# Optimization experiments

Hardware: AMD Instinct MI355X
Metric: run time of the kernel (lower is better)

Reference implementation:

```python
import jax, jax.numpy as jnp
import numpy as np

B, S, H, HEADS = 4, 4096, 256, 4
DH = H // HEADS
WINDOW = 16
N = B * S
EPS = 1e-5


def _build_edges():
    half = WINDOW // 2
    i = np.arange(S)
    offs = np.concatenate([np.arange(-half, 0), np.arange(1, half)])  # j in [i-half, i+half), j != i
    j = i[:, None] + offs[None, :]
    valid = (j >= 0) & (j < S)
    src_i = np.broadcast_to(i[:, None], j.shape)[valid]
    tgt_j = j[valid]
    w = (1.0 / (1.0 + np.abs(src_i - tgt_j))).astype(np.float32)
    boff = np.arange(B)[:, None] * S
    src = (boff + src_i[None, :]).reshape(-1).astype(np.int32)
    tgt = (boff + tgt_j[None, :]).reshape(-1).astype(np.int32)
    w = np.tile(w, B)
    return src, tgt, w


def setup_inputs() -> dict:
    key = jax.random.key(0)
    ks = jax.random.split(key, 8)
    src, tgt, w = _build_edges()
    sc = 0.02
    return {
        "hidden_states": jax.random.normal(ks[0], (B, S, H), jnp.float32),
        "Wc": jax.random.normal(ks[1], (H, H), jnp.float32) * sc,
        "bc": jnp.zeros((H,), jnp.float32),
        "Wa": jax.random.normal(ks[2], (H, H), jnp.float32) * sc,
        "a_src": jax.random.normal(ks[3], (HEADS, DH), jnp.float32) * sc,
        "a_tgt": jax.random.normal(ks[4], (HEADS, DH), jnp.float32) * sc,
        "ba": jnp.zeros((H,), jnp.float32),
        "ln_g": jnp.ones((H,), jnp.float32),
        "ln_b": jnp.zeros((H,), jnp.float32),
        "Wg": jax.random.normal(ks[5], (2 * H, H), jnp.float32) * sc,
        "bg": jnp.zeros((H,), jnp.float32),
        "Wp": jax.random.normal(ks[6], (H, H), jnp.float32) * sc,
        "bp": jnp.zeros((H,), jnp.float32),
        "edge_weights": jnp.asarray(w),
        "src": jnp.asarray(src),
        "tgt": jnp.asarray(tgt),
    }


def _ln(x, g, b):
    mu = jnp.mean(x, -1, keepdims=True)
    var = jnp.mean((x - mu) ** 2, -1, keepdims=True)
    return (x - mu) * jax.lax.rsqrt(var + EPS) * g + b


def reference(hidden_states, Wc, bc, Wa, a_src, a_tgt, ba, ln_g, ln_b,
              Wg, bg, Wp, bp, edge_weights, src, tgt):
    x = hidden_states.reshape(N, H)

    # --- layer 0: GraphConvolution ---
    support = x @ Wc                                   # [N,H]
    msg = edge_weights[:, None] * support[src]         # [E,H]
    gs = jax.ops.segment_sum(msg, tgt, num_segments=N) + bc
    gs = _ln(gs + x, ln_g, ln_b)

    # --- layer 1: GraphAttention (GAT-style, edge-weighted softmax) ---
    h = (gs @ Wa).reshape(N, HEADS, DH)
    es = jnp.einsum('nhd,hd->nh', h, a_src)            # [N,heads]
    et = jnp.einsum('nhd,hd->nh', h, a_tgt)
    logits = jax.nn.leaky_relu(es[src] + et[tgt], 0.2)  # [E,heads]
    m = jax.ops.segment_max(logits, tgt, num_segments=N)
    un = jnp.exp(logits - m[tgt]) * edge_weights[:, None]
    den = jax.ops.segment_sum(un, tgt, num_segments=N)
    alpha = un / (den[tgt] + 1e-9)                      # [E,heads]
    agg = jax.ops.segment_sum(alpha[:, :, None] * h[src], tgt, num_segments=N)
    gs = agg.reshape(N, H) + ba
    gs = _ln(gs + x, ln_g, ln_b)

    # --- gated integration ---
    gate = jax.nn.sigmoid(jnp.concatenate([x, gs], -1) @ Wg + bg)
    enhanced = x + gate * (gs @ Wp + bp)
    return enhanced.reshape(B, S, H)
```

## Files before the change

kernel.cpp:

```cpp
#include <hip/hip_runtime.h>
#include <math.h>

#define HD 256
#define SEQ 4096
#define NR 16384
#define NHEADS 4
#define EPSV 1e-5f
#define LDP 72
#define SROWS 32
#define SHALO 15
#define SLDP 264

typedef __attribute__((ext_vector_type(8))) short bf16x8;
typedef __attribute__((ext_vector_type(4))) float f32x4;

__device__ inline short f2bf(float f) {
    unsigned u = __float_as_uint(f);
    u += 0x7FFF + ((u >> 16) & 1);
    return (short)(u >> 16);
}
__device__ inline float bf2f(short s) {
    return __uint_as_float(((unsigned)(unsigned short)s) << 16);
}

__device__ inline void stage_tile(const short* __restrict__ src, int src_stride,
                                  int row0, int k0, short* lds, int rows)
{
    int t = threadIdx.x;
    int nchunk = rows >> 5;
#pragma unroll
    for (int c = 0; c < 4; ++c) {
        if (c >= nchunk) break;
        int idx = c * 256 + t;
        int r = idx >> 3, kg = idx & 7;
        bf16x8 v = *(const bf16x8*)(src + (size_t)(row0 + r) * src_stride + k0 + kg * 8);
        *(bf16x8*)(lds + r * LDP + kg * 8) = v;
    }
}

__device__ inline void stage_tile_ln(const short* __restrict__ z, int row0, int k0,
                                     const float* __restrict__ musum,
                                     const float* __restrict__ sqsum,
                                     const float* __restrict__ g,
                                     const float* __restrict__ b,
                                     short* lds, int rows)
{
    int t = threadIdx.x;
    int nchunk = rows >> 5;
#pragma unroll
    for (int c = 0; c < 4; ++c) {
        if (c >= nchunk) break;
        int idx = c * 256 + t;
        int r = idx >> 3, kg = idx & 7;
        int row = row0 + r;
        float s = musum[row], q = sqsum[row];
        float mu = s * (1.f / HD);
        float inv = rsqrtf(q * (1.f / HD) - mu * mu + EPSV);
        bf16x8 v = *(const bf16x8*)(z + (size_t)row * HD + k0 + kg * 8);
        float4 g0 = *(const float4*)(g + k0 + kg * 8);
        float4 g1 = *(const float4*)(g + k0 + kg * 8 + 4);
        float4 b0 = *(const float4*)(b + k0 + kg * 8);
        float4 b1 = *(const float4*)(b + k0 + kg * 8 + 4);
        bf16x8 o;
        o[0] = f2bf((bf2f(v[0]) - mu) * inv * g0.x + b0.x);
        o[1] = f2bf((bf2f(v[1]) - mu) * inv * g0.y + b0.y);
        o[2] = f2bf((bf2f(v[2]) - mu) * inv * g0.z + b0.z);
        o[3] = f2bf((bf2f(v[3]) - mu) * inv * g0.w + b0.w);
        o[4] = f2bf((bf2f(v[4]) - mu) * inv * g1.x + b1.x);
        o[5] = f2bf((bf2f(v[5]) - mu) * inv * g1.y + b1.y);
        o[6] = f2bf((bf2f(v[6]) - mu) * inv * g1.z + b1.z);
        o[7] = f2bf((bf2f(v[7]) - mu) * inv * g1.w + b1.w);
        *(bf16x8*)(lds + r * LDP + kg * 8) = o;
    }
}

__global__ __launch_bounds__(256) void prep_stencil(
    const float* __restrict__ x,
    const float* __restrict__ Wc, const float* __restrict__ Wa,
    const float* __restrict__ Wg, const float* __restrict__ Wp,
    short* __restrict__ xb, short* __restrict__ y,
    short* __restrict__ WcT, short* __restrict__ WaT,
    short* __restrict__ WgT, short* __restrict__ WpT,
    float* __restrict__ musum, float* __restrict__ sqsum)
{
    __shared__ __align__(16) char smem[(SROWS + SHALO) * SLDP * 2];
    int task = blockIdx.y;
    int bx = blockIdx.x;
    int t = threadIdx.x;

    if (task == 0) {
        short* lH = (short*)smem;
        int t0 = bx * SROWS;
        int batch_base = t0 & ~(SEQ - 1);
        for (int i = t; i < (SROWS + SHALO) * 64; i += 256) {
            int r = i >> 6, c4 = (i & 63) * 4;
            int grow = t0 - 7 + r;
            short4 o4 = {0, 0, 0, 0};
            if (grow >= batch_base && grow < batch_base + SEQ) {
                float4 v = *(const float4*)(x + (size_t)grow * HD + c4);
                o4.x = f2bf(v.x); o4.y = f2bf(v.y); o4.z = f2bf(v.z); o4.w = f2bf(v.w);
            }
            *(short4*)(lH + r * SLDP + c4) = o4;
        }
        __syncthreads();
        for (int i = t; i < SROWS * 64; i += 256) {
            int r = i >> 6, c4 = (i & 63) * 4;
            *(short4*)(xb + (size_t)(t0 + r) * HD + c4) =
                *(const short4*)(lH + (r + 7) * SLDP + c4);
        }
        int wv = t >> 6, lane = t & 63;
        int c0 = lane * 4;
        for (int rr = wv; rr < SROWS; rr += 4) {
            float a0 = 0.f, a1 = 0.f, a2 = 0.f, a3 = 0.f;
#pragma unroll
            for (int i = 0; i < 15; ++i) {
                int d = (i < 7) ? (i - 7) : (i - 6);
                float wd = 1.f / (1.f + (float)((d < 0) ? -d : d));
                short4 s4 = *(const short4*)(lH + (rr + 7 + d) * SLDP + c0);
                a0 += wd * bf2f(s4.x); a1 += wd * bf2f(s4.y);
                a2 += wd * bf2f(s4.z); a3 += wd * bf2f(s4.w);
            }
            short4 o;
            o.x = f2bf(a0); o.y = f2bf(a1); o.z = f2bf(a2); o.w = f2bf(a3);
            *(short4*)(y + (size_t)(t0 + rr) * HD + c0) = o;
        }
        return;
    }
    if (task == 5) {
        int idx = bx * 256 + t;
        if (idx < NR) { musum[idx] = 0.f; sqsum[idx] = 0.f; }
        return;
    }
    float (*lds)[65] = (float (*)[65])smem;
    const float* W; short* Wt; int K;
    if (task == 1)      { W = Wc; Wt = WcT; K = 256; }
    else if (task == 2) { W = Wa; Wt = WaT; K = 256; }
    else if (task == 3) { W = Wg; Wt = WgT; K = 512; }
    else                { W = Wp; Wt = WpT; K = 256; }
    int ntiles = (K >> 6) * 4;
    if (bx >= ntiles) return;
    int k0 = (bx >> 2) * 64, n0 = (bx & 3) * 64;
    int ty = t >> 6, tx = t & 63;
#pragma unroll
    for (int s = 0; s < 16; ++s) {
        int r = s * 4 + ty;
        lds[r][tx] = W[(size_t)(k0 + r) * 256 + n0 + tx];
    }
    __syncthreads();
#pragma unroll
    for (int s = 0; s < 16; ++s) {
        int rn = s * 4 + ty;
        Wt[(size_t)(n0 + rn) * K + k0 + tx] = f2bf(lds[tx][rn]);
    }
}

__global__ __launch_bounds__(256) void gemm1z(const short* __restrict__ A,
                                              const short* __restrict__ BT,
                                              const short* __restrict__ xb,
                                              const float* __restrict__ bc,
                                              short* __restrict__ Z,
                                              float* __restrict__ musum,
                                              float* __restrict__ sqsum)
{
    __shared__ __align__(16) short lA[64 * LDP];
    __shared__ __align__(16) short lB[64 * LDP];
    int tid = threadIdx.x;
    int lane = tid & 63, wid = tid >> 6;
    int m0 = blockIdx.y * 64;
    int n0 = blockIdx.x * 64;
    int wrow = wid * 16;
    int lm = lane & 15, lk = (lane >> 4) * 8;
    f32x4 acc[4] = {};
    for (int kt = 0; kt < 4; ++kt) {
        __syncthreads();
        stage_tile(A,  HD, m0, kt * 64, lA, 64);
        stage_tile(BT, HD, n0, kt * 64, lB, 64);
        __syncthreads();
#pragma unroll
        for (int kk2 = 0; kk2 < 64; kk2 += 32) {
            bf16x8 a = *(const bf16x8*)(lA + (wrow + lm) * LDP + kk2 + lk);
            bf16x8 b[4];
#pragma unroll
            for (int j = 0; j < 4; ++j)
                b[j] = *(const bf16x8*)(lB + (j * 16 + lm) * LDP + kk2 + lk);
#pragma unroll
            for (int j = 0; j < 4; ++j)
                acc[j] = __builtin_amdgcn_mfma_f32_16x16x32_bf16(a, b[j], acc[j], 0, 0, 0);
        }
    }
    int rbase = (lane >> 4) * 4;
#pragma unroll
    for (int r = 0; r < 4; ++r) {
        int row = m0 + wrow + rbase + r;
        float s = 0.f, q = 0.f;
#pragma unroll
        for (int j = 0; j < 4; ++j) {
            int n = n0 + j * 16 + lm;
            float z = acc[j][r] + bc[n] + bf2f(xb[(size_t)row * HD + n]);
            Z[(size_t)row * HD + n] = f2bf(z);
            s += z; q += z * z;
        }
#pragma unroll
        for (int o = 1; o < 16; o <<= 1) {
            s += __shfl_xor(s, o, 64);
            q += __shfl_xor(q, o, 64);
        }
        if (lm == 0) {
            atomicAdd(&musum[row], s);
            atomicAdd(&sqsum[row], q);
        }
    }
}

__global__ __launch_bounds__(256) void gemm_dots2(const short* __restrict__ Z,
                                                  const short* __restrict__ BT,
                                                  const float* __restrict__ musum,
                                                  const float* __restrict__ sqsum,
                                                  const float* __restrict__ lng,
                                                  const float* __restrict__ lnb,
                                                  const float* __restrict__ a_src,
                                                  const float* __restrict__ a_tgt,
                                                  short* __restrict__ C,
                                                  float* __restrict__ es,
                                                  float* __restrict__ et)
{
    __shared__ __align__(16) short lA[64 * LDP];
    __shared__ __align__(16) short lB[64 * LDP];
    int tid = threadIdx.x;
    int lane = tid & 63, wid = tid >> 6;
    int m0 = blockIdx.y * 64;
    int n0 = blockIdx.x * 64;
    int wrow = wid * 16;
    int lm = lane & 15, lk = (lane >> 4) * 8;
    f32x4 acc[4] = {};
    for (int kt = 0; kt < 4; ++kt) {
        __syncthreads();
        stage_tile_ln(Z, m0, kt * 64, musum, sqsum, lng, lnb, lA, 64);
        stage_tile(BT, HD, n0, kt * 64, lB, 64);
        __syncthreads();
#pragma unroll
        for (int kk2 = 0; kk2 < 64; kk2 += 32) {
            bf16x8 a = *(const bf16x8*)(lA + (wrow + lm) * LDP + kk2 + lk);
            bf16x8 b[4];
#pragma unroll
            for (int j = 0; j < 4; ++j)
                b[j] = *(const bf16x8*)(lB + (j * 16 + lm) * LDP + kk2 + lk);
#pragma unroll
            for (int j = 0; j < 4; ++j)
                acc[j] = __builtin_amdgcn_mfma_f32_16x16x32_bf16(a, b[j], acc[j], 0, 0, 0);
        }
    }
    int rbase = (lane >> 4) * 4;
#pragma unroll
    for (int j = 0; j < 4; ++j)
#pragma unroll
        for (int r = 0; r < 4; ++r)
            C[(size_t)(m0 + wrow + rbase + r) * HD + n0 + j * 16 + lm] = f2bf(acc[j][r]);

    float as4[4], at4[4];
#pragma unroll
    for (int j = 0; j < 4; ++j) {
        as4[j] = a_src[n0 + j * 16 + lm];
        at4[j] = a_tgt[n0 + j * 16 + lm];
    }
#pragma unroll
    for (int r = 0; r < 4; ++r) {
        float ps = 0.f, pt = 0.f;
#pragma unroll
        for (int j = 0; j < 4; ++j) {
            ps += acc[j][r] * as4[j];
            pt += acc[j][r] * at4[j];
        }
#pragma unroll
        for (int o = 1; o < 16; o <<= 1) {
            ps += __shfl_xor(ps, o, 64);
            pt += __shfl_xor(pt, o, 64);
        }
        if (lm == 0) {
            int row = m0 + wrow + rbase + r;
            es[row * NHEADS + blockIdx.x] = ps;
            et[row * NHEADS + blockIdx.x] = pt;
        }
    }
}

__global__ __launch_bounds__(256) void attn_ln(const short* __restrict__ hb,
                                               const float* __restrict__ es,
                                               const float* __restrict__ et,
                                               const short* __restrict__ xb,
                                               const float* __restrict__ ba,
                                               const float* __restrict__ g,
                                               const float* __restrict__ bb,
                                               short* __restrict__ out)
{
    __shared__ short lH[(SROWS + SHALO) * SLDP];
    int t0 = blockIdx.x * SROWS;
    int batch_base = t0 & ~(SEQ - 1);
    int t = threadIdx.x;
    for (int i = t; i < (SROWS + SHALO) * 64; i += 256) {
        int r = i >> 6, c4 = (i & 63) * 4;
        int grow = t0 - 7 + r;
        short4 v = {0, 0, 0, 0};
        if (grow >= batch_base && grow < batch_base + SEQ)
            v = *(const short4*)(hb + (size_t)grow * HD + c4);
        *(short4*)(lH + r * SLDP + c4) = v;
    }
    __syncthreads();

    int wv = t >> 6, lane = t & 63;
    int tap = lane >> 2, hh = lane & 3;
    int hd = lane >> 4;
    int c0 = lane * 4;
    for (int rr = wv; rr < SROWS; rr += 4) {
        int trow = t0 + rr;
        int p = trow & (SEQ - 1);
        float lg = -1e30f, wd = 0.f;
        bool okk = false;
        if (tap < 15) {
            int d = (tap < 7) ? (tap - 7) : (tap - 6);
            int qp = p + d;
            okk = (qp >= 0) && (qp < SEQ);
            if (okk) {
                float l = es[(trow + d) * NHEADS + hh] + et[trow * NHEADS + hh];
                lg = (l > 0.f) ? l : 0.2f * l;
            }
            wd = 1.f / (1.f + (float)((d < 0) ? -d : d));
        }
        float m = lg;
#pragma unroll
        for (int o = 4; o < 64; o <<= 1) m = fmaxf(m, __shfl_xor(m, o, 64));
        float un = okk ? __expf(lg - m) * wd : 0.f;
        float den = un;
#pragma unroll
        for (int o = 4; o < 64; o <<= 1) den += __shfl_xor(den, o, 64);
        float alpha_l = un / (den + 1e-9f);

        float al[15];
#pragma unroll
        for (int i = 0; i < 15; ++i) al[i] = __shfl(alpha_l, i * 4 + hd, 64);

        float a0 = 0.f, a1 = 0.f, a2 = 0.f, a3 = 0.f;
#pragma unroll
        for (int i = 0; i < 15; ++i) {
            int d = (i < 7) ? (i - 7) : (i - 6);
            short4 s4 = *(const short4*)(lH + (rr + 7 + d) * SLDP + c0);
            a0 += al[i] * bf2f(s4.x); a1 += al[i] * bf2f(s4.y);
            a2 += al[i] * bf2f(s4.z); a3 += al[i] * bf2f(s4.w);
        }
        short4 xv4 = *(const short4*)(xb + (size_t)trow * HD + c0);
        float4 bav = *(const float4*)(ba + c0);
        float v0 = a0 + bav.x + bf2f(xv4.x), v1 = a1 + bav.y + bf2f(xv4.y);
        float v2 = a2 + bav.z + bf2f(xv4.z), v3 = a3 + bav.w + bf2f(xv4.w);
        float s = v0 + v1 + v2 + v3;
        float q = v0 * v0 + v1 * v1 + v2 * v2 + v3 * v3;
#pragma unroll
        for (int o = 1; o < 64; o <<= 1) { s += __shfl_xor(s, o, 64); q += __shfl_xor(q, o, 64); }
        float mu = s * (1.f / HD);
        float var = q * (1.f / HD) - mu * mu;
        float inv = rsqrtf(var + EPSV);
        float4 gv = *(const float4*)(g + c0);
        float4 bv = *(const float4*)(bb + c0);
        short4 o4;
        o4.x = f2bf((v0 - mu) * inv * gv.x + bv.x);
        o4.y = f2bf((v1 - mu) * inv * gv.y + bv.y);
        o4.z = f2bf((v2 - mu) * inv * gv.z + bv.z);
        o4.w = f2bf((v3 - mu) * inv * gv.w + bv.w);
        *(short4*)(out + (size_t)trow * HD + c0) = o4;
    }
}

__global__ __launch_bounds__(256) void final_mfma(const short* __restrict__ xb,
                                                  const short* __restrict__ gs2b,
                                                  const short* __restrict__ WgT,
                                                  const float* __restrict__ bg,
                                                  const short* __restrict__ WpT,
                                                  const float* __restrict__ bp,
                                                  float* __restrict__ out)
{
    __shared__ __align__(16) short lX[64 * LDP];
    __shared__ __align__(16) short lG[64 * LDP];
    __shared__ __align__(16) short lB1[64 * LDP];
    __shared__ __align__(16) short lB2[64 * LDP];
    __shared__ __align__(16) short lB3[64 * LDP];
    int tid = threadIdx.x;
    int lane = tid & 63, wid = tid >> 6;
    int m0 = blockIdx.y * 64;
    int n0 = blockIdx.x * 64;
    int wrow = wid * 16;
    int lm = lane & 15, lk = (lane >> 4) * 8;
    f32x4 accg[4] = {}, accp[4] = {};
    for (int kt = 0; kt < 4; ++kt) {
        int k0 = kt * 64;
        __syncthreads();
        stage_tile(xb,   HD,  m0, k0, lX, 64);
        stage_tile(gs2b, HD,  m0, k0, lG, 64);
        stage_tile(WgT,  512, n0, k0, lB1, 64);
        stage_tile(WgT,  512, n0, k0 + 256, lB2, 64);
        stage_tile(WpT,  HD,  n0, k0, lB3, 64);
        __syncthreads();
#pragma unroll
        for (int kk2 = 0; kk2 < 64; kk2 += 32) {
            int ro = (wrow + lm) * LDP + kk2 + lk;
            bf16x8 ax = *(const bf16x8*)(lX + ro);
            bf16x8 ag = *(const bf16x8*)(lG + ro);
            bf16x8 b1[4], b2[4], b3[4];
#pragma unroll
            for (int j = 0; j < 4; ++j) {
                int rb = (j * 16 + lm) * LDP + kk2 + lk;
                b1[j] = *(const bf16x8*)(lB1 + rb);
                b2[j] = *(const bf16x8*)(lB2 + rb);
                b3[j] = *(const bf16x8*)(lB3 + rb);
            }
#pragma unroll
            for (int j = 0; j < 4; ++j) {
                accg[j] = __builtin_amdgcn_mfma_f32_16x16x32_bf16(ax, b1[j], accg[j], 0, 0, 0);
                accg[j] = __builtin_amdgcn_mfma_f32_16x16x32_bf16(ag, b2[j], accg[j], 0, 0, 0);
                accp[j] = __builtin_amdgcn_mfma_f32_16x16x32_bf16(ag, b3[j], accp[j], 0, 0, 0);
            }
        }
    }
    int rbase = (lane >> 4) * 4;
#pragma unroll
    for (int j = 0; j < 4; ++j)
#pragma unroll
        for (int r = 0; r < 4; ++r) {
            size_t m = (size_t)(m0 + wrow + rbase + r);
            int n = n0 + j * 16 + lm;
            float gate = 1.f / (1.f + __expf(-(accg[j][r] + bg[n])));
            float pv = accp[j][r] + bp[n];
            out[m * HD + n] = bf2f(xb[m * HD + n]) + gate * pv;
        }
}

extern "C" void kernel_launch(void* const* d_in, const int* in_sizes, int n_in,
                              void* d_out, int out_size, void* d_ws, size_t ws_size,
                              hipStream_t stream)
{
    const float* x     = (const float*)d_in[0];
    const float* Wc    = (const float*)d_in[1];
    const float* bc    = (const float*)d_in[2];
    const float* Wa    = (const float*)d_in[3];
    const float* a_src = (const float*)d_in[4];
    const float* a_tgt = (const float*)d_in[5];
    const float* ba    = (const float*)d_in[6];
    const float* ln_g  = (const float*)d_in[7];
    const float* ln_b  = (const float*)d_in[8];
    const float* Wg    = (const float*)d_in[9];
    const float* bg    = (const float*)d_in[10];
    const float* Wp    = (const float*)d_in[11];
    const float* bp    = (const float*)d_in[12];

    float* out = (float*)d_out;
    short* hb  = (short*)d_out;
    char* dsec = (char*)d_out + (size_t)NR * HD * 2;
    float* es  = (float*)dsec;
    float* et  = es + (size_t)NR * NHEADS;

    char* w = (char*)d_ws;
    short* y   = (short*)w;   w += (size_t)NR * HD * 2;
    short* zb  = (short*)w;   w += (size_t)NR * HD * 2;
    short* xb  = (short*)w;   w += (size_t)NR * HD * 2;
    short* WcT = (short*)w;   w += 256 * 256 * 2;
    short* WaT = (short*)w;   w += 256 * 256 * 2;
    short* WpT = (short*)w;   w += 256 * 256 * 2;
    short* WgT = (short*)w;   w += 512 * 256 * 2;
    float* musum = (float*)w; w += (size_t)NR * 4;
    float* sqsum = (float*)w; w += (size_t)NR * 4;

    dim3 ggrid(HD / 64, NR / 64);

    prep_stencil<<<dim3(NR / SROWS, 6), 256, 0, stream>>>(
        x, Wc, Wa, Wg, Wp, xb, y, WcT, WaT, WgT, WpT, musum, sqsum);
    gemm1z<<<ggrid, 256, 0, stream>>>(y, WcT, xb, bc, zb, musum, sqsum);
    gemm_dots2<<<ggrid, 256, 0, stream>>>(zb, WaT, musum, sqsum, ln_g, ln_b,
                                          a_src, a_tgt, hb, es, et);
    attn_ln<<<NR / SROWS, 256, 0, stream>>>(hb, es, et, xb, ba, ln_g, ln_b, zb);
    final_mfma<<<ggrid, 256, 0, stream>>>(xb, zb, WgT, bg, WpT, bp, out);
}
```

Baseline: 81.36 us.

## Fuse GCN GEMM, LayerNorm and attention GEMM into one full-row kernel

```diff
diff --git a/kernel.cpp b/kernel.cpp
--- a/kernel.cpp
+++ b/kernel.cpp
@@ -7,6 +7,7 @@
 #define NHEADS 4
 #define EPSV 1e-5f
 #define LDP 72
+#define ZLDP 264
 #define SROWS 32
 #define SHALO 15
 #define SLDP 264
@@ -29,48 +30,12 @@
     int t = threadIdx.x;
     int nchunk = rows >> 5;
 #pragma unroll
-    for (int c = 0; c < 4; ++c) {
+    for (int c = 0; c < 8; ++c) {
         if (c >= nchunk) break;
         int idx = c * 256 + t;
         int r = idx >> 3, kg = idx & 7;
         bf16x8 v = *(const bf16x8*)(src + (size_t)(row0 + r) * src_stride + k0 + kg * 8);
         *(bf16x8*)(lds + r * LDP + kg * 8) = v;
-    }
-}
-
-__device__ inline void stage_tile_ln(const short* __restrict__ z, int row0, int k0,
-                                     const float* __restrict__ musum,
-                                     const float* __restrict__ sqsum,
-                                     const float* __restrict__ g,
-                                     const float* __restrict__ b,
-                                     short* lds, int rows)
-{
-    int t = threadIdx.x;
-    int nchunk = rows >> 5;
-#pragma unroll
-    for (int c = 0; c < 4; ++c) {
-        if (c >= nchunk) break;
-        int idx = c * 256 + t;
-        int r = idx >> 3, kg = idx & 7;
-        int row = row0 + r;
-        float s = musum[row], q = sqsum[row];
-        float mu = s * (1.f / HD);
-        float inv = rsqrtf(q * (1.f / HD) - mu * mu + EPSV);
-        bf16x8 v = *(const bf16x8*)(z + (size_t)row * HD + k0 + kg * 8);
-        float4 g0 = *(const float4*)(g + k0 + kg * 8);
-        float4 g1 = *(const float4*)(g + k0 + kg * 8 + 4);
-        float4 b0 = *(const float4*)(b + k0 + kg * 8);
-        float4 b1 = *(const float4*)(b + k0 + kg * 8 + 4);
-        bf16x8 o;
-        o[0] = f2bf((bf2f(v[0]) - mu) * inv * g0.x + b0.x);
-        o[1] = f2bf((bf2f(v[1]) - mu) * inv * g0.y + b0.y);
-        o[2] = f2bf((bf2f(v[2]) - mu) * inv * g0.z + b0.z);
-        o[3] = f2bf((bf2f(v[3]) - mu) * inv * g0.w + b0.w);
-        o[4] = f2bf((bf2f(v[4]) - mu) * inv * g1.x + b1.x);
-        o[5] = f2bf((bf2f(v[5]) - mu) * inv * g1.y + b1.y);
-        o[6] = f2bf((bf2f(v[6]) - mu) * inv * g1.z + b1.z);
-        o[7] = f2bf((bf2f(v[7]) - mu) * inv * g1.w + b1.w);
-        *(bf16x8*)(lds + r * LDP + kg * 8) = o;
     }
 }
 
@@ -80,8 +45,7 @@
     const float* __restrict__ Wg, const float* __restrict__ Wp,
     short* __restrict__ xb, short* __restrict__ y,
     short* __restrict__ WcT, short* __restrict__ WaT,
-    short* __restrict__ WgT, short* __restrict__ WpT,
-    float* __restrict__ musum, float* __restrict__ sqsum)
+    short* __restrict__ WgT, short* __restrict__ WpT)
 {
     __shared__ __align__(16) char smem[(SROWS + SHALO) * SLDP * 2];
     int task = blockIdx.y;
@@ -126,11 +90,6 @@
         }
         return;
     }
-    if (task == 5) {
-        int idx = bx * 256 + t;
-        if (idx < NR) { musum[idx] = 0.f; sqsum[idx] = 0.f; }
-        return;
-    }
     float (*lds)[65] = (float (*)[65])smem;
     const float* W; short* Wt; int K;
     if (task == 1)      { W = Wc; Wt = WcT; K = 256; }
@@ -154,132 +113,131 @@
     }
 }
 
-__global__ __launch_bounds__(256) void gemm1z(const short* __restrict__ A,
-                                              const short* __restrict__ BT,
-                                              const short* __restrict__ xb,
-                                              const float* __restrict__ bc,
-                                              short* __restrict__ Z,
-                                              float* __restrict__ musum,
-                                              float* __restrict__ sqsum)
-{
-    __shared__ __align__(16) short lA[64 * LDP];
-    __shared__ __align__(16) short lB[64 * LDP];
-    int tid = threadIdx.x;
-    int lane = tid & 63, wid = tid >> 6;
-    int m0 = blockIdx.y * 64;
-    int n0 = blockIdx.x * 64;
-    int wrow = wid * 16;
+__global__ __launch_bounds__(256) void gemm_fused(
+    const short* __restrict__ y, const short* __restrict__ WcT,
+    const short* __restrict__ xb, const float* __restrict__ bc,
+    const short* __restrict__ WaT,
+    const float* __restrict__ lng, const float* __restrict__ lnb,
+    const float* __restrict__ a_src, const float* __restrict__ a_tgt,
+    short* __restrict__ hb, float* __restrict__ es, float* __restrict__ et)
+{
+    __shared__ __align__(16) short lA[32 * LDP];
+    __shared__ __align__(16) short lB[256 * LDP];
+    __shared__ __align__(16) short lZ[32 * ZLDP];
+    __shared__ float red_s[2][32], red_q[2][32];
+    int t = threadIdx.x;
+    int lane = t & 63, wid = t >> 6;
+    int wm = wid & 1, wn = wid >> 1;
+    int m0 = blockIdx.x * 32;
     int lm = lane & 15, lk = (lane >> 4) * 8;
-    f32x4 acc[4] = {};
+    int rbase = (lane >> 4) * 4;
+
+    f32x4 acc[8] = {};
     for (int kt = 0; kt < 4; ++kt) {
         __syncthreads();
-        stage_tile(A,  HD, m0, kt * 64, lA, 64);
-        stage_tile(BT, HD, n0, kt * 64, lB, 64);
+        {
+            int r = t >> 3, kg = t & 7;
+            *(bf16x8*)(lA + r * LDP + kg * 8) =
+                *(const bf16x8*)(y + (size_t)(m0 + r) * HD + kt * 64 + kg * 8);
+        }
+        stage_tile(WcT, HD, 0, kt * 64, lB, 256);
         __syncthreads();
 #pragma unroll
         for (int kk2 = 0; kk2 < 64; kk2 += 32) {
-            bf16x8 a = *(const bf16x8*)(lA + (wrow + lm) * LDP + kk2 + lk);
-            bf16x8 b[4];
-#pragma unroll
-            for (int j = 0; j < 4; ++j)
-                b[j] = *(const bf16x8*)(lB + (j * 16 + lm) * LDP + kk2 + lk);
-#pragma unroll
-            for (int j = 0; j < 4; ++j)
-                acc[j] = __builtin_amdgcn_mfma_f32_16x16x32_bf16(a, b[j], acc[j], 0, 0, 0);
-        }
-    }
-    int rbase = (lane >> 4) * 4;
+            bf16x8 a = *(const bf16x8*)(lA + (wm * 16 + lm) * LDP + kk2 + lk);
+#pragma unroll
+            for (int j = 0; j < 8; ++j) {
+                bf16x8 b = *(const bf16x8*)(lB + (wn * 128 + j * 16 + lm) * LDP + kk2 + lk);
+                acc[j] = __builtin_amdgcn_mfma_f32_16x16x32_bf16(a, b, acc[j], 0, 0, 0);
+            }
+        }
+    }
+    float zv[8][4];
+    float s4r[4] = {}, q4r[4] = {};
+#pragma unroll
+    for (int j = 0; j < 8; ++j)
+#pragma unroll
+        for (int r = 0; r < 4; ++r) {
+            int n = wn * 128 + j * 16 + lm;
+            int row = m0 + wm * 16 + rbase + r;
+            float z = acc[j][r] + bc[n] + bf2f(xb[(size_t)row * HD + n]);
+            zv[j][r] = z; s4r[r] += z; q4r[r] += z * z;
+        }
+#pragma unroll
+    for (int r = 0; r < 4; ++r)
+#pragma unroll
+        for (int o = 1; o < 16; o <<= 1) {
+            s4r[r] += __shfl_xor(s4r[r], o, 64);
+            q4r[r] += __shfl_xor(q4r[r], o, 64);
+        }
+    if (lm == 0)
+#pragma unroll
+        for (int r = 0; r < 4; ++r) {
+            red_s[wn][wm * 16 + rbase + r] = s4r[r];
+            red_q[wn][wm * 16 + rbase + r] = q4r[r];
+        }
+    __syncthreads();
+    float mu[4], inv[4];
 #pragma unroll
     for (int r = 0; r < 4; ++r) {
-        int row = m0 + wrow + rbase + r;
-        float s = 0.f, q = 0.f;
-#pragma unroll
-        for (int j = 0; j < 4; ++j) {
-            int n = n0 + j * 16 + lm;
-            float z = acc[j][r] + bc[n] + bf2f(xb[(size_t)row * HD + n]);
-            Z[(size_t)row * HD + n] = f2bf(z);
-            s += z; q += z * z;
-        }
+        int rowl = wm * 16 + rbase + r;
+        float S = red_s[0][rowl] + red_s[1][rowl];
+        float Q = red_q[0][rowl] + red_q[1][rowl];
+        mu[r] = S * (1.f / HD);
+        inv[r] = rsqrtf(Q * (1.f / HD) - mu[r] * mu[r] + EPSV);
+    }
+#pragma unroll
+    for (int j = 0; j < 8; ++j)
+#pragma unroll
+        for (int r = 0; r < 4; ++r) {
+            int n = wn * 128 + j * 16 + lm;
+            int rowl = wm * 16 + rbase + r;
+            lZ[rowl * ZLDP + n] = f2bf((zv[j][r] - mu[r]) * inv[r] * lng[n] + lnb[n]);
+        }
+
+    f32x4 acc2[8] = {};
+    for (int kt = 0; kt < 4; ++kt) {
+        __syncthreads();
+        stage_tile(WaT, HD, 0, kt * 64, lB, 256);
+        __syncthreads();
+#pragma unroll
+        for (int kk2 = 0; kk2 < 64; kk2 += 32) {
+            bf16x8 a = *(const bf16x8*)(lZ + (wm * 16 + lm) * ZLDP + kt * 64 + kk2 + lk);
+#pragma unroll
+            for (int j = 0; j < 8; ++j) {
+                bf16x8 b = *(const bf16x8*)(lB + (wn * 128 + j * 16 + lm) * LDP + kk2 + lk);
+                acc2[j] = __builtin_amdgcn_mfma_f32_16x16x32_bf16(a, b, acc2[j], 0, 0, 0);
+            }
+        }
+    }
+    float esA[4] = {}, etA[4] = {}, esB[4] = {}, etB[4] = {};
+#pragma unroll
+    for (int j = 0; j < 8; ++j) {
+        int n = wn * 128 + j * 16 + lm;
+        float as = a_src[n], at = a_tgt[n];
+#pragma unroll
+        for (int r = 0; r < 4; ++r) {
+            int row = m0 + wm * 16 + rbase + r;
+            hb[(size_t)row * HD + n] = f2bf(acc2[j][r]);
+            if (j < 4) { esA[r] += acc2[j][r] * as; etA[r] += acc2[j][r] * at; }
+            else       { esB[r] += acc2[j][r] * as; etB[r] += acc2[j][r] * at; }
+        }
+    }
+#pragma unroll
+    for (int r = 0; r < 4; ++r) {
 #pragma unroll
         for (int o = 1; o < 16; o <<= 1) {
-            s += __shfl_xor(s, o, 64);
-            q += __shfl_xor(q, o, 64);
+            esA[r] += __shfl_xor(esA[r], o, 64);
+            etA[r] += __shfl_xor(etA[r], o, 64);
+            esB[r] += __shfl_xor(esB[r], o, 64);
+            etB[r] += __shfl_xor(etB[r], o, 64);
         }
         if (lm == 0) {
-            atomicAdd(&musum[row], s);
-            atomicAdd(&sqsum[row], q);
-        }
-    }
-}
-
-__global__ __launch_bounds__(256) void gemm_dots2(const short* __restrict__ Z,
-                                                  const short* __restrict__ BT,
-                                                  const float* __restrict__ musum,
-                                                  const float* __restrict__ sqsum,
-                                                  const float* __restrict__ lng,
-                                                  const float* __restrict__ lnb,
-                                                  const float* __restrict__ a_src,
-                                                  const float* __restrict__ a_tgt,
-                                                  short* __restrict__ C,
-                                                  float* __restrict__ es,
-                                                  float* __restrict__ et)
-{
-    __shared__ __align__(16) short lA[64 * LDP];
-    __shared__ __align__(16) short lB[64 * LDP];
-    int tid = threadIdx.x;
-    int lane = tid & 63, wid = tid >> 6;
-    int m0 = blockIdx.y * 64;
-    int n0 = blockIdx.x * 64;
-    int wrow = wid * 16;
-    int lm = lane & 15, lk = (lane >> 4) * 8;
-    f32x4 acc[4] = {};
-    for (int kt = 0; kt < 4; ++kt) {
-        __syncthreads();
-        stage_tile_ln(Z, m0, kt * 64, musum, sqsum, lng, lnb, lA, 64);
-        stage_tile(BT, HD, n0, kt * 64, lB, 64);
-        __syncthreads();
-#pragma unroll
-        for (int kk2 = 0; kk2 < 64; kk2 += 32) {
-            bf16x8 a = *(const bf16x8*)(lA + (wrow + lm) * LDP + kk2 + lk);
-            bf16x8 b[4];
-#pragma unroll
-            for (int j = 0; j < 4; ++j)
-                b[j] = *(const bf16x8*)(lB + (j * 16 + lm) * LDP + kk2 + lk);
-#pragma unroll
-            for (int j = 0; j < 4; ++j)
-                acc[j] = __builtin_amdgcn_mfma_f32_16x16x32_bf16(a, b[j], acc[j], 0, 0, 0);
-        }
-    }
-    int rbase = (lane >> 4) * 4;
-#pragma unroll
-    for (int j = 0; j < 4; ++j)
-#pragma unroll
-        for (int r = 0; r < 4; ++r)
-            C[(size_t)(m0 + wrow + rbase + r) * HD + n0 + j * 16 + lm] = f2bf(acc[j][r]);
-
-    float as4[4], at4[4];
-#pragma unroll
-    for (int j = 0; j < 4; ++j) {
-        as4[j] = a_src[n0 + j * 16 + lm];
-        at4[j] = a_tgt[n0 + j * 16 + lm];
-    }
-#pragma unroll
-    for (int r = 0; r < 4; ++r) {
-        float ps = 0.f, pt = 0.f;
-#pragma unroll
-        for (int j = 0; j < 4; ++j) {
-            ps += acc[j][r] * as4[j];
-            pt += acc[j][r] * at4[j];
-        }
-#pragma unroll
-        for (int o = 1; o < 16; o <<= 1) {
-            ps += __shfl_xor(ps, o, 64);
-            pt += __shfl_xor(pt, o, 64);
-        }
-        if (lm == 0) {
-            int row = m0 + wrow + rbase + r;
-            es[row * NHEADS + blockIdx.x] = ps;
-            et[row * NHEADS + blockIdx.x] = pt;
+            int row = m0 + wm * 16 + rbase + r;
+            es[row * NHEADS + wn * 2 + 0] = esA[r];
+            et[row * NHEADS + wn * 2 + 0] = etA[r];
+            es[row * NHEADS + wn * 2 + 1] = esB[r];
+            et[row * NHEADS + wn * 2 + 1] = etB[r];
         }
     }
 }
@@ -458,22 +416,19 @@
 
     char* w = (char*)d_ws;
     short* y   = (short*)w;   w += (size_t)NR * HD * 2;
-    short* zb  = (short*)w;   w += (size_t)NR * HD * 2;
+    short* gsb = (short*)w;   w += (size_t)NR * HD * 2;
     short* xb  = (short*)w;   w += (size_t)NR * HD * 2;
     short* WcT = (short*)w;   w += 256 * 256 * 2;
     short* WaT = (short*)w;   w += 256 * 256 * 2;
     short* WpT = (short*)w;   w += 256 * 256 * 2;
     short* WgT = (short*)w;   w += 512 * 256 * 2;
-    float* musum = (float*)w; w += (size_t)NR * 4;
-    float* sqsum = (float*)w; w += (size_t)NR * 4;
 
     dim3 ggrid(HD / 64, NR / 64);
 
-    prep_stencil<<<dim3(NR / SROWS, 6), 256, 0, stream>>>(
-        x, Wc, Wa, Wg, Wp, xb, y, WcT, WaT, WgT, WpT, musum, sqsum);
-    gemm1z<<<ggrid, 256, 0, stream>>>(y, WcT, xb, bc, zb, musum, sqsum);
-    gemm_dots2<<<ggrid, 256, 0, stream>>>(zb, WaT, musum, sqsum, ln_g, ln_b,
-                                          a_src, a_tgt, hb, es, et);
-    attn_ln<<<NR / SROWS, 256, 0, stream>>>(hb, es, et, xb, ba, ln_g, ln_b, zb);
-    final_mfma<<<ggrid, 256, 0, stream>>>(xb, zb, WgT, bg, WpT, bp, out);
-}
+    prep_stencil<<<dim3(NR / SROWS, 5), 256, 0, stream>>>(
+        x, Wc, Wa, Wg, Wp, xb, y, WcT, WaT, WgT, WpT);
+    gemm_fused<<<NR / 32, 256, 0, stream>>>(y, WcT, xb, bc, WaT, ln_g, ln_b,
+                                            a_src, a_tgt, hb, es, et);
+    attn_ln<<<NR / SROWS, 256, 0, stream>>>(hb, es, et, xb, ba, ln_g, ln_b, gsb);
+    final_mfma<<<ggrid, 256, 0, stream>>>(xb, gsb, WgT, bg, WpT, bp, out);
+}
```

Result: faster. 69.87 us (-14.1%).
